# Kernel tuning notes

Hardware: AMD Instinct MI355X
Metric: run time of the kernel (lower is better)

## Reference

```python
import jax, jax.numpy as jnp
import numpy as np

FEATURES_M = 1_000_000
HIDDEN = 64
LAYERS = [128, 64]
BATCH = 16384
N_FIELDS = 50


def setup_inputs() -> dict:
    key = jax.random.key(0)
    ks = jax.random.split(key, 12)
    inp = {
        "features": jax.random.randint(ks[0], (BATCH, N_FIELDS), 0, FEATURES_M, dtype=jnp.int32),
        "labels": jax.random.normal(ks[1], (BATCH, 1), dtype=jnp.float32),
        # learned parameters
        "emb_table": jax.random.normal(ks[2], (FEATURES_M, HIDDEN), dtype=jnp.float32) * 0.01,
        "bias_table": jax.random.normal(ks[3], (FEATURES_M, 1), dtype=jnp.float32) * 0.01,
        "w_bias": jax.random.normal(ks[4], (1, 1), dtype=jnp.float32),  # Dense(1, use_bias=False)
        "W1": jax.random.normal(ks[5], (HIDDEN, LAYERS[0]), dtype=jnp.float32) * (1.0 / np.sqrt(HIDDEN)),
        "b1": jnp.zeros((LAYERS[0],), dtype=jnp.float32),
        "W2": jax.random.normal(ks[6], (LAYERS[0], LAYERS[1]), dtype=jnp.float32) * (1.0 / np.sqrt(LAYERS[0])),
        "b2": jnp.zeros((LAYERS[1],), dtype=jnp.float32),
        "Wp": jax.random.normal(ks[7], (LAYERS[1], 1), dtype=jnp.float32) * (1.0 / np.sqrt(LAYERS[1])),
        "bp": jnp.zeros((1,), dtype=jnp.float32),
    }
    return inp


def reference(features, labels, emb_table, bias_table, w_bias, W1, b1, W2, b2, Wp, bp):
    # Embedding gather: [B, F, D]
    nonzero_emb = emb_table[features]
    # FM bi-interaction pooling: 0.5 * ((sum e)^2 - sum(e^2))  -> [B, D]
    summed = jnp.sum(nonzero_emb, axis=1)
    squared_sum = jnp.sum(jnp.square(nonzero_emb), axis=1)
    fm = 0.5 * (jnp.square(summed) - squared_sum)
    # Deep MLP stack (batch_norm off, dropout identity at eval keep_prob=1)
    h = jax.nn.relu(fm @ W1 + b1)
    h = jax.nn.relu(h @ W2 + b2)
    pred = h @ Wp + bp  # [B, 1]
    bilinear = jnp.sum(pred, axis=1, keepdims=True)  # [B, 1]
    # First-order feature bias: gather [B, F, 1] then sum over fields
    feature_bias = jnp.sum(bias_table[features], axis=1)  # [B, 1]
    # Global bias: Dense(1, no bias) applied to ones_like(labels)
    global_bias = jnp.ones_like(labels) @ w_bias  # [B, 1]
    return bilinear + feature_bias + global_bias
```

## Files before the change

### kernel.cpp

```cpp
#include <hip/hip_runtime.h>


#define NFIELDS 50
#define HIDDEN  64
#define L1N     128
#define L2N     64
#define RPW     4
#define WAVES   4
#define ROWS_PER_BLOCK (RPW * WAVES)

__global__ __launch_bounds__(256, 4) void neuralfm_kernel(
    const int*   __restrict__ features,
    const float* __restrict__ emb,
    const float* __restrict__ bias_t,
    const float* __restrict__ w_bias,
    const float* __restrict__ W1,
    const float* __restrict__ b1,
    const float* __restrict__ W2,
    const float* __restrict__ b2,
    const float* __restrict__ Wp,
    const float* __restrict__ bp,
    float*       __restrict__ out)
{
    __shared__ int    sIdx[WAVES][RPW * NFIELDS];
    __shared__ float4 sFm4[WAVES][RPW * HIDDEN / 4];
    __shared__ float  sH1 [WAVES][RPW * L1N];

    const int tid  = threadIdx.x;
    const int wave = tid >> 6;
    const int lane = tid & 63;
    const int sub  = lane >> 4;
    const int le   = lane & 15;
    const int row0 = blockIdx.x * ROWS_PER_BLOCK + wave * RPW;

    const int idx_base = row0 * NFIELDS;
    #pragma unroll
    for (int t = lane; t < RPW * NFIELDS; t += 64)
        sIdx[wave][t] = features[idx_base + t];
    __syncthreads();

    float biasacc[RPW];
    #pragma unroll
    for (int r = 0; r < RPW; ++r) biasacc[r] = 0.f;
    if (lane < NFIELDS) {
        #pragma unroll
        for (int r = 0; r < RPW; ++r)
            biasacc[r] = bias_t[sIdx[wave][r * NFIELDS + lane]];
    }

    const float4* __restrict__ emb4 = (const float4*)emb;
    float sx = 0.f, sy = 0.f, sz = 0.f, sw = 0.f;
    float qx = 0.f, qy = 0.f, qz = 0.f, qw = 0.f;
    const int* myIdx = &sIdx[wave][sub * NFIELDS];
    #pragma unroll
    for (int f = 0; f < NFIELDS; ++f) {
        const int    idx = myIdx[f];
        const float4 v   = emb4[(size_t)idx * (HIDDEN / 4) + le];
        sx += v.x; sy += v.y; sz += v.z; sw += v.w;
        qx += v.x * v.x; qy += v.y * v.y; qz += v.z * v.z; qw += v.w * v.w;
    }
    float4 fm;
    fm.x = 0.5f * (sx * sx - qx);
    fm.y = 0.5f * (sy * sy - qy);
    fm.z = 0.5f * (sz * sz - qz);
    fm.w = 0.5f * (sw * sw - qw);
    sFm4[wave][sub * (HIDDEN / 4) + le] = fm;
    __syncthreads();

    float h1a[RPW], h1b[RPW];
    #pragma unroll
    for (int r = 0; r < RPW; ++r) { h1a[r] = 0.f; h1b[r] = 0.f; }

    for (int dq = 0; dq < HIDDEN / 4; ++dq) {
        float w0[4], w1[4];
        #pragma unroll
        for (int c = 0; c < 4; ++c) {
            w0[c] = W1[(4 * dq + c) * L1N + lane];
            w1[c] = W1[(4 * dq + c) * L1N + 64 + lane];
        }
        #pragma unroll
        for (int r = 0; r < RPW; ++r) {
            const float4 fv = sFm4[wave][r * (HIDDEN / 4) + dq];
            h1a[r] += fv.x * w0[0] + fv.y * w0[1] + fv.z * w0[2] + fv.w * w0[3];
            h1b[r] += fv.x * w1[0] + fv.y * w1[1] + fv.z * w1[2] + fv.w * w1[3];
        }
    }
    const float bias1a = b1[lane];
    const float bias1b = b1[64 + lane];
    #pragma unroll
    for (int r = 0; r < RPW; ++r) {
        sH1[wave][r * L1N + lane]      = fmaxf(h1a[r] + bias1a, 0.f);
        sH1[wave][r * L1N + 64 + lane] = fmaxf(h1b[r] + bias1b, 0.f);
    }
    __syncthreads();

    const float4* sH14 = (const float4*)&sH1[wave][0];
    float h2[RPW];
    #pragma unroll
    for (int r = 0; r < RPW; ++r) h2[r] = 0.f;

    for (int jq = 0; jq < L1N / 4; ++jq) {
        float w[4];
        #pragma unroll
        for (int c = 0; c < 4; ++c)
            w[c] = W2[(4 * jq + c) * L2N + lane];
        #pragma unroll
        for (int r = 0; r < RPW; ++r) {
            const float4 hv = sH14[r * (L1N / 4) + jq];
            h2[r] += hv.x * w[0] + hv.y * w[1] + hv.z * w[2] + hv.w * w[3];
        }
    }
    const float bias2 = b2[lane];
    const float wp    = Wp[lane];

    float tot[RPW];
    #pragma unroll
    for (int r = 0; r < RPW; ++r)
        tot[r] = fmaxf(h2[r] + bias2, 0.f) * wp + biasacc[r];

    #pragma unroll
    for (int r = 0; r < RPW; ++r) {
        float v = tot[r];
        #pragma unroll
        for (int off = 32; off > 0; off >>= 1)
            v += __shfl_xor(v, off, 64);
        tot[r] = v;
    }
    if (lane == 0) {
        const float c = bp[0] + w_bias[0];
        #pragma unroll
        for (int r = 0; r < RPW; ++r)
            out[row0 + r] = tot[r] + c;
    }
}

extern "C" void kernel_launch(void* const* d_in, const int* in_sizes, int n_in,
                              void* d_out, int out_size, void* d_ws, size_t ws_size,
                              hipStream_t stream) {
    const int*   features = (const int*)  d_in[0];
    const float* emb      = (const float*)d_in[2];
    const float* bias_t   = (const float*)d_in[3];
    const float* w_bias   = (const float*)d_in[4];
    const float* W1       = (const float*)d_in[5];
    const float* b1       = (const float*)d_in[6];
    const float* W2       = (const float*)d_in[7];
    const float* b2       = (const float*)d_in[8];
    const float* Wp       = (const float*)d_in[9];
    const float* bp       = (const float*)d_in[10];
    float*       out      = (float*)d_out;

    const int batch  = in_sizes[0] / NFIELDS;
    const int blocks = batch / ROWS_PER_BLOCK;

    neuralfm_kernel<<<blocks, 256, 0, stream>>>(
        features, emb, bias_t, w_bias, W1, b1, W2, b2, Wp, bp, out);
}
```

Before: 353.9 us.

## Use single-wave blocks, 32-bit gather offsets, float2 W1 loads, parallel output store

Shrinks each block from four waves to one, so __syncthreads only covers one wave and blocks finish on their own with less shared memory each. The embedding gather now computes a 32-bit byte offset instead of a 64-bit index multiply. The W1 loads become float2 with each lane owning two adjacent output columns, and four lanes write the outputs in parallel. The trade-off is four times as many blocks and more scheduling overhead per block, and the 32-bit offset only holds while the table stays under 4 GiB.

```diff
diff --git a/kernel.cpp b/kernel.cpp
--- a/kernel.cpp
+++ b/kernel.cpp
@@ -6,10 +6,8 @@
 #define L1N     128
 #define L2N     64
 #define RPW     4
-#define WAVES   4
-#define ROWS_PER_BLOCK (RPW * WAVES)
 
-__global__ __launch_bounds__(256, 4) void neuralfm_kernel(
+__global__ __launch_bounds__(64, 4) void neuralfm_kernel(
     const int*   __restrict__ features,
     const float* __restrict__ emb,
     const float* __restrict__ bias_t,
@@ -22,21 +20,19 @@
     const float* __restrict__ bp,
     float*       __restrict__ out)
 {
-    __shared__ int    sIdx[WAVES][RPW * NFIELDS];
-    __shared__ float4 sFm4[WAVES][RPW * HIDDEN / 4];
-    __shared__ float  sH1 [WAVES][RPW * L1N];
+    __shared__ int    sIdx[RPW * NFIELDS];
+    __shared__ float4 sFm4[RPW * HIDDEN / 4];
+    __shared__ float  sH1 [RPW * L1N];
 
-    const int tid  = threadIdx.x;
-    const int wave = tid >> 6;
-    const int lane = tid & 63;
+    const int lane = threadIdx.x;
     const int sub  = lane >> 4;
     const int le   = lane & 15;
-    const int row0 = blockIdx.x * ROWS_PER_BLOCK + wave * RPW;
+    const int row0 = blockIdx.x * RPW;
 
     const int idx_base = row0 * NFIELDS;
     #pragma unroll
     for (int t = lane; t < RPW * NFIELDS; t += 64)
-        sIdx[wave][t] = features[idx_base + t];
+        sIdx[t] = features[idx_base + t];
     __syncthreads();
 
     float biasacc[RPW];
@@ -45,17 +41,18 @@
     if (lane < NFIELDS) {
         #pragma unroll
         for (int r = 0; r < RPW; ++r)
-            biasacc[r] = bias_t[sIdx[wave][r * NFIELDS + lane]];
+            biasacc[r] = bias_t[sIdx[r * NFIELDS + lane]];
     }
 
-    const float4* __restrict__ emb4 = (const float4*)emb;
+    const char* __restrict__ embB = (const char*)emb;
+    const unsigned leoff = (unsigned)(le * 16);
     float sx = 0.f, sy = 0.f, sz = 0.f, sw = 0.f;
     float qx = 0.f, qy = 0.f, qz = 0.f, qw = 0.f;
-    const int* myIdx = &sIdx[wave][sub * NFIELDS];
+    const int* myIdx = &sIdx[sub * NFIELDS];
     #pragma unroll
     for (int f = 0; f < NFIELDS; ++f) {
-        const int    idx = myIdx[f];
-        const float4 v   = emb4[(size_t)idx * (HIDDEN / 4) + le];
+        const unsigned off = (unsigned)myIdx[f] * 256u + leoff;
+        const float4 v = *(const float4*)(embB + off);
         sx += v.x; sy += v.y; sz += v.z; sw += v.w;
         qx += v.x * v.x; qy += v.y * v.y; qz += v.z * v.z; qw += v.w * v.w;
     }
@@ -64,37 +61,37 @@
     fm.y = 0.5f * (sy * sy - qy);
     fm.z = 0.5f * (sz * sz - qz);
     fm.w = 0.5f * (sw * sw - qw);
-    sFm4[wave][sub * (HIDDEN / 4) + le] = fm;
+    sFm4[sub * (HIDDEN / 4) + le] = fm;
     __syncthreads();
 
-    float h1a[RPW], h1b[RPW];
+    float h1x[RPW], h1y[RPW];
     #pragma unroll
-    for (int r = 0; r < RPW; ++r) { h1a[r] = 0.f; h1b[r] = 0.f; }
+    for (int r = 0; r < RPW; ++r) { h1x[r] = 0.f; h1y[r] = 0.f; }
+    const int n0 = 2 * lane;
 
     for (int dq = 0; dq < HIDDEN / 4; ++dq) {
-        float w0[4], w1[4];
+        float2 w[4];
         #pragma unroll
-        for (int c = 0; c < 4; ++c) {
-            w0[c] = W1[(4 * dq + c) * L1N + lane];
-            w1[c] = W1[(4 * dq + c) * L1N + 64 + lane];
-        }
+        for (int c = 0; c < 4; ++c)
+            w[c] = *(const float2*)&W1[(4 * dq + c) * L1N + n0];
         #pragma unroll
         for (int r = 0; r < RPW; ++r) {
-            const float4 fv = sFm4[wave][r * (HIDDEN / 4) + dq];
-            h1a[r] += fv.x * w0[0] + fv.y * w0[1] + fv.z * w0[2] + fv.w * w0[3];
-            h1b[r] += fv.x * w1[0] + fv.y * w1[1] + fv.z * w1[2] + fv.w * w1[3];
+            const float4 fv = sFm4[r * (HIDDEN / 4) + dq];
+            h1x[r] += fv.x * w[0].x + fv.y * w[1].x + fv.z * w[2].x + fv.w * w[3].x;
+            h1y[r] += fv.x * w[0].y + fv.y * w[1].y + fv.z * w[2].y + fv.w * w[3].y;
         }
     }
-    const float bias1a = b1[lane];
-    const float bias1b = b1[64 + lane];
+    const float2 b1v = *(const float2*)&b1[n0];
     #pragma unroll
     for (int r = 0; r < RPW; ++r) {
-        sH1[wave][r * L1N + lane]      = fmaxf(h1a[r] + bias1a, 0.f);
-        sH1[wave][r * L1N + 64 + lane] = fmaxf(h1b[r] + bias1b, 0.f);
+        float2 hv;
+        hv.x = fmaxf(h1x[r] + b1v.x, 0.f);
+        hv.y = fmaxf(h1y[r] + b1v.y, 0.f);
+        *(float2*)&sH1[r * L1N + n0] = hv;
     }
     __syncthreads();
 
-    const float4* sH14 = (const float4*)&sH1[wave][0];
+    const float4* sH14 = (const float4*)sH1;
     float h2[RPW];
     #pragma unroll
     for (int r = 0; r < RPW; ++r) h2[r] = 0.f;
@@ -126,11 +123,12 @@
             v += __shfl_xor(v, off, 64);
         tot[r] = v;
     }
-    if (lane == 0) {
-        const float c = bp[0] + w_bias[0];
-        #pragma unroll
-        for (int r = 0; r < RPW; ++r)
-            out[row0 + r] = tot[r] + c;
+    if (lane < RPW) {
+        float v = tot[0];
+        v = (lane == 1) ? tot[1] : v;
+        v = (lane == 2) ? tot[2] : v;
+        v = (lane == 3) ? tot[3] : v;
+        out[row0 + lane] = v + bp[0] + w_bias[0];
     }
 }
 
@@ -150,8 +148,8 @@
     float*       out      = (float*)d_out;
 
     const int batch  = in_sizes[0] / NFIELDS;
-    const int blocks = batch / ROWS_PER_BLOCK;
+    const int blocks = batch / RPW;
 
-    neuralfm_kernel<<<blocks, 256, 0, stream>>>(
+    neuralfm_kernel<<<blocks, 64, 0, stream>>>(
         features, emb, bias_t, w_bias, W1, b1, W2, b2, Wp, bp, out);
 }
```

After: 356.1 us. Within noise of the previous version (+0.6%).
